# Kernel optimization log

Measured on AMD Instinct MI355X. Metric: run time of the kernel, lower is better.

## Reference

```python
import jax, jax.numpy as jnp
import numpy as np

INPUT_DIM = 256
RES_DIM = 2048
OUT_DIM = 256
BATCH = 32
SEQ = 512
LEAK = 0.3
TARGET_SR = 0.9
IN_CONN = 0.1
RES_CONN = 0.1
IN_SCALE = 1.0


def _make_params(seed=0):
    rng = np.random.default_rng(seed)
    W_in = rng.standard_normal((RES_DIM, INPUT_DIM)).astype(np.float32)
    W_in = W_in * (rng.random((RES_DIM, INPUT_DIM)) < IN_CONN).astype(np.float32) * IN_SCALE
    W = rng.standard_normal((RES_DIM, RES_DIM)).astype(np.float32)
    W = W * (rng.random((RES_DIM, RES_DIM)) < RES_CONN).astype(np.float32)
    sr = np.abs(np.linalg.eigvals(W.astype(np.float64))).max()
    if sr > 0:
        W = (W * (TARGET_SR / sr)).astype(np.float32)
    bias = np.zeros((RES_DIM,), np.float32)
    # readout Linear(reservoir_dim, output_dim), torch default init
    bound = 1.0 / np.sqrt(RES_DIM)
    w_ro = rng.uniform(-bound, bound, (OUT_DIM, RES_DIM)).astype(np.float32)
    b_ro = rng.uniform(-bound, bound, (OUT_DIM,)).astype(np.float32)
    return W_in, W, bias, w_ro, b_ro


def setup_inputs() -> dict:
    key = jax.random.key(0)
    k_u, _ = jax.random.split(key)
    u = jax.random.normal(k_u, (BATCH, SEQ, INPUT_DIM), dtype=jnp.float32)
    state = jnp.zeros((BATCH, RES_DIM), dtype=jnp.float32)
    W_in, W, bias, w_ro, b_ro = _make_params()
    return {
        'u': u,
        'state': state,
        'W_in': jnp.asarray(W_in),
        'W': jnp.asarray(W),
        'bias': jnp.asarray(bias),
        'w_ro': jnp.asarray(w_ro),
        'b_ro': jnp.asarray(b_ro),
    }


def reference(u, state, W_in, W, bias, w_ro, b_ro):
    # Precompute input projection for all timesteps in one GEMM: (T, B, R)
    u_proj = jnp.einsum('bti,ri->tbr', u, W_in) + bias

    def step(s, up):
        pre = up + s @ W.T            # (B, R)
        s = (1.0 - LEAK) * s + LEAK * jnp.tanh(pre)
        return s, s

    _, states = jax.lax.scan(step, state, u_proj)  # (T, B, R)
    states = jnp.transpose(states, (1, 0, 2))       # (B, T, R)
    output = jnp.einsum('btr,or->bto', states, w_ro) + b_ro
    return output
```

## Files before the change

kernel.cpp:

```cpp
#include <hip/hip_runtime.h>
#include <math.h>

#define BATCH 32
#define SEQ   512
#define IDIM  256
#define RDIM  2048
#define ODIM  256
#define LEAK  0.3f

#define SCAN_BLOCKS  256
#define SCAN_THREADS 512
#define ROWS_PER_BLK 8

typedef float f4 __attribute__((ext_vector_type(4)));

__device__ __forceinline__ unsigned ld_flag(const unsigned* p) {
    return __hip_atomic_load(p, __ATOMIC_RELAXED, __HIP_MEMORY_SCOPE_AGENT);
}
__device__ __forceinline__ void st_flag(unsigned* p, unsigned v) {
    __hip_atomic_store(p, v, __ATOMIC_RELAXED, __HIP_MEMORY_SCOPE_AGENT);
}

__global__ void esn_init(const float* __restrict__ s0, float* __restrict__ states,
                         unsigned* __restrict__ flags) {
    int idx = blockIdx.x * blockDim.x + threadIdx.x;
    const int n4 = (BATCH * RDIM) / 4;
    if (idx < n4) {
        ((float4*)states)[idx] = ((const float4*)s0)[idx];
    }
    if (idx < 512) flags[idx] = 0u;
}

#define UP_THREADS 256
__global__ __launch_bounds__(UP_THREADS) void esn_uproj(
    const float* __restrict__ u,
    const float* __restrict__ Win,
    const float* __restrict__ bias,
    float* __restrict__ up)
{
    __shared__ float St[32][68];
    __shared__ float Wt[32][68];

    const int tid  = threadIdx.x;
    const int row0 = blockIdx.x * 64;
    const int o0   = blockIdx.y * 64;

    const int lr = tid >> 3;
    const int lk = (tid & 7) * 4;
    const int tx = tid & 15;
    const int ty = tid >> 4;

    const int m0 = row0 + lr;
    const int m1 = row0 + 32 + lr;
    const float* u0 = u + ((size_t)(m0 & 31) * SEQ + (m0 >> 5)) * IDIM;
    const float* u1 = u + ((size_t)(m1 & 31) * SEQ + (m1 >> 5)) * IDIM;

    float acc[4][4] = {};

    for (int kt = 0; kt < IDIM; kt += 32) {
        float4 a0 = *(const float4*)(u0 + kt + lk);
        float4 a1 = *(const float4*)(u1 + kt + lk);
        float4 w0 = *(const float4*)(Win + (size_t)(o0 + lr)      * IDIM + kt + lk);
        float4 w1 = *(const float4*)(Win + (size_t)(o0 + 32 + lr) * IDIM + kt + lk);
        __syncthreads();
        float av0[4] = {a0.x, a0.y, a0.z, a0.w};
        float av1[4] = {a1.x, a1.y, a1.z, a1.w};
        float wv0[4] = {w0.x, w0.y, w0.z, w0.w};
        float wv1[4] = {w1.x, w1.y, w1.z, w1.w};
        #pragma unroll
        for (int j = 0; j < 4; ++j) {
            St[lk + j][lr]      = av0[j];
            St[lk + j][32 + lr] = av1[j];
            Wt[lk + j][lr]      = wv0[j];
            Wt[lk + j][32 + lr] = wv1[j];
        }
        __syncthreads();
        #pragma unroll
        for (int k = 0; k < 32; ++k) {
            float4 a4 = *(const float4*)(&St[k][4 * ty]);
            float4 b4 = *(const float4*)(&Wt[k][4 * tx]);
            float av[4] = {a4.x, a4.y, a4.z, a4.w};
            float bv[4] = {b4.x, b4.y, b4.z, b4.w};
            #pragma unroll
            for (int ri = 0; ri < 4; ++ri)
                #pragma unroll
                for (int oi = 0; oi < 4; ++oi)
                    acc[ri][oi] += av[ri] * bv[oi];
        }
    }

    float4 bs = *(const float4*)(bias + o0 + 4 * tx);
    float bsv[4] = {bs.x, bs.y, bs.z, bs.w};
    #pragma unroll
    for (int ri = 0; ri < 4; ++ri) {
        int row = row0 + 4 * ty + ri;
        float4 v;
        v.x = acc[ri][0] + bsv[0];
        v.y = acc[ri][1] + bsv[1];
        v.z = acc[ri][2] + bsv[2];
        v.w = acc[ri][3] + bsv[3];
        *(float4*)(up + (size_t)row * RDIM + o0 + 4 * tx) = v;
    }
}

#define DECL_A(r)  float A##r##0 = 0.0f, A##r##1 = 0.0f, A##r##2 = 0.0f, A##r##3 = 0.0f;
#define ZERO_A(r)  A##r##0 = 0.0f; A##r##1 = 0.0f; A##r##2 = 0.0f; A##r##3 = 0.0f;
#define DOT_ROW(r) { f4 w = *(const f4*)(wl + (r) * RDIM); \
    A##r##0 += w[0]*SC0[0] + w[1]*SC0[1] + w[2]*SC0[2] + w[3]*SC0[3]; \
    A##r##1 += w[0]*SC1[0] + w[1]*SC1[1] + w[2]*SC1[2] + w[3]*SC1[3]; \
    A##r##2 += w[0]*SC2[0] + w[1]*SC2[1] + w[2]*SC2[2] + w[3]*SC2[3]; \
    A##r##3 += w[0]*SC3[0] + w[1]*SC3[1] + w[2]*SC3[2] + w[3]*SC3[3]; }
#define RED12(x)   { x += __shfl_xor(x, 1, 64); x += __shfl_xor(x, 2, 64); }
#define RED_A(r)   RED12(A##r##0) RED12(A##r##1) RED12(A##r##2) RED12(A##r##3)
#define COMPACT(r) float V##r; { \
    float x01 = (q & 1) ? A##r##1 : A##r##0; \
    float x23 = (q & 1) ? A##r##3 : A##r##2; \
    float v   = (q & 2) ? x23 : x01; \
    v += __shfl_xor(v, 4, 64);  v += __shfl_xor(v, 8, 64); \
    v += __shfl_xor(v, 16, 64); v += __shfl_xor(v, 32, 64); \
    V##r = v; }

__global__ __launch_bounds__(SCAN_THREADS) void esn_scan(
    const float* __restrict__ W,
    float* __restrict__ states,
    unsigned* __restrict__ flags)
{
    __shared__ float Wl[ROWS_PER_BLK * RDIM];

    const int tid  = threadIdx.x;
    const int bid  = blockIdx.x;
    const int r0   = bid * ROWS_PER_BLK;
    unsigned* go   = flags + 320;

    {
        const float4* src = (const float4*)(W + (size_t)r0 * RDIM);
        float4* dst = (float4*)Wl;
        #pragma unroll
        for (int i = 0; i < (ROWS_PER_BLK * RDIM) / 4 / SCAN_THREADS; ++i)
            dst[i * SCAN_THREADS + tid] = src[i * SCAN_THREADS + tid];
    }

    const int wave = tid >> 6;
    const int lane = tid & 63;
    const int b0   = wave * 4;
    const int kb   = lane * 4;
    const int q    = lane & 3;

    const int bf = b0 + q;
    const int rr = lane >> 2;
    const size_t fin_off = (size_t)bf * RDIM + r0 + rr;

    float so = 0.0f;
    if (lane < 32) so = states[fin_off];

    DECL_A(0) DECL_A(1) DECL_A(2) DECL_A(3)
    DECL_A(4) DECL_A(5) DECL_A(6) DECL_A(7)

    __syncthreads();

    for (int t = 0; t < SEQ; ++t) {
        const float* prev = states + (size_t)t * (BATCH * RDIM);
        float* next = states + (size_t)(t + 1) * (BATCH * RDIM);

        float up = 0.0f;
        if (lane < 32)
            up = __hip_atomic_load(&next[fin_off], __ATOMIC_RELAXED,
                                   __HIP_MEMORY_SCOPE_AGENT);

        ZERO_A(0) ZERO_A(1) ZERO_A(2) ZERO_A(3)
        ZERO_A(4) ZERO_A(5) ZERO_A(6) ZERO_A(7)

        {
            const float* sb = prev + kb;
            f4 SC0 = *(const f4*)(sb + (size_t)(b0 + 0) * RDIM);
            f4 SC1 = *(const f4*)(sb + (size_t)(b0 + 1) * RDIM);
            f4 SC2 = *(const f4*)(sb + (size_t)(b0 + 2) * RDIM);
            f4 SC3 = *(const f4*)(sb + (size_t)(b0 + 3) * RDIM);

            #pragma unroll 1
            for (int c = 0; c < 8; ++c) {
                f4 SN0 = SC0, SN1 = SC1, SN2 = SC2, SN3 = SC3;
                if (c < 7) {
                    SN0 = *(const f4*)(sb + (size_t)(b0 + 0) * RDIM + (c + 1) * 256);
                    SN1 = *(const f4*)(sb + (size_t)(b0 + 1) * RDIM + (c + 1) * 256);
                    SN2 = *(const f4*)(sb + (size_t)(b0 + 2) * RDIM + (c + 1) * 256);
                    SN3 = *(const f4*)(sb + (size_t)(b0 + 3) * RDIM + (c + 1) * 256);
                }
                const float* wl = &Wl[c * 256 + kb];
                DOT_ROW(0) DOT_ROW(1) DOT_ROW(2) DOT_ROW(3)
                DOT_ROW(4) DOT_ROW(5) DOT_ROW(6) DOT_ROW(7)
                SC0 = SN0; SC1 = SN1; SC2 = SN2; SC3 = SN3;
            }
        }

        RED_A(0) RED_A(1) RED_A(2) RED_A(3)
        RED_A(4) RED_A(5) RED_A(6) RED_A(7)
        COMPACT(0) COMPACT(1) COMPACT(2) COMPACT(3)
        COMPACT(4) COMPACT(5) COMPACT(6) COMPACT(7)

        if (lane < 32) {
            float pre = V0;
            if (rr == 1) pre = V1;
            if (rr == 2) pre = V2;
            if (rr == 3) pre = V3;
            if (rr == 4) pre = V4;
            if (rr == 5) pre = V5;
            if (rr == 6) pre = V6;
            if (rr == 7) pre = V7;
            pre += up;
            float sn = (1.0f - LEAK) * so + LEAK * tanhf(pre);
            so = sn;
            __hip_atomic_store(&next[fin_off], sn,
                               __ATOMIC_RELAXED, __HIP_MEMORY_SCOPE_AGENT);
        }

        asm volatile("s_waitcnt vmcnt(0)" ::: "memory");
        __syncthreads();
        if (tid == 0) st_flag(&flags[bid], (unsigned)(t + 1));
        asm volatile("" ::: "memory");

        const unsigned tp = (unsigned)(t + 1);
        if (bid == 0) {
            if (tid < 64) {
                for (;;) {
                    unsigned f0 = ld_flag(&flags[tid]);
                    unsigned f1 = ld_flag(&flags[64 + tid]);
                    unsigned f2 = ld_flag(&flags[128 + tid]);
                    unsigned f3 = ld_flag(&flags[192 + tid]);
                    bool ok = (f0 >= tp) & (f1 >= tp) & (f2 >= tp) & (f3 >= tp);
                    if (__all(ok)) break;
                    __builtin_amdgcn_s_sleep(2);
                }
                asm volatile("" ::: "memory");
                if (tid == 0) st_flag(go, tp);
            }
        } else {
            if (tid == 0) {
                while (ld_flag(go) < tp) __builtin_amdgcn_s_sleep(2);
            }
        }
        __syncthreads();
    }
}

#define RO_THREADS 256
__global__ __launch_bounds__(RO_THREADS) void esn_readout(
    const float* __restrict__ states,
    const float* __restrict__ w_ro,
    const float* __restrict__ b_ro,
    float* __restrict__ out)
{
    __shared__ float St[32][68];
    __shared__ float Wt[32][68];

    const int tid  = threadIdx.x;
    const int rb   = blockIdx.x >> 2;
    const int ob   = blockIdx.x & 3;
    const int row0 = rb * 64;
    const int o0   = ob * 64;
    const float* S = states + (size_t)BATCH * RDIM;

    const int lr = tid >> 3;
    const int lk = (tid & 7) * 4;
    const int tx = tid & 15;
    const int ty = tid >> 4;

    float acc[4][4] = {};

    for (int kt = 0; kt < RDIM; kt += 32) {
        float4 a0 = *(const float4*)(S + (size_t)(row0 + lr)      * RDIM + kt + lk);
        float4 a1 = *(const float4*)(S + (size_t)(row0 + 32 + lr) * RDIM + kt + lk);
        float4 w0 = *(const float4*)(w_ro + (size_t)(o0 + lr)      * RDIM + kt + lk);
        float4 w1 = *(const float4*)(w_ro + (size_t)(o0 + 32 + lr) * RDIM + kt + lk);
        __syncthreads();
        float av0[4] = {a0.x, a0.y, a0.z, a0.w};
        float av1[4] = {a1.x, a1.y, a1.z, a1.w};
        float wv0[4] = {w0.x, w0.y, w0.z, w0.w};
        float wv1[4] = {w1.x, w1.y, w1.z, w1.w};
        #pragma unroll
        for (int j = 0; j < 4; ++j) {
            St[lk + j][lr]      = av0[j];
            St[lk + j][32 + lr] = av1[j];
            Wt[lk + j][lr]      = wv0[j];
            Wt[lk + j][32 + lr] = wv1[j];
        }
        __syncthreads();
        #pragma unroll
        for (int k = 0; k < 32; ++k) {
            float4 a4 = *(const float4*)(&St[k][4 * ty]);
            float4 b4 = *(const float4*)(&Wt[k][4 * tx]);
            float av[4] = {a4.x, a4.y, a4.z, a4.w};
            float bv[4] = {b4.x, b4.y, b4.z, b4.w};
            #pragma unroll
            for (int ri = 0; ri < 4; ++ri)
                #pragma unroll
                for (int oi = 0; oi < 4; ++oi)
                    acc[ri][oi] += av[ri] * bv[oi];
        }
    }

    float4 br = *(const float4*)(b_ro + o0 + 4 * tx);
    float brv[4] = {br.x, br.y, br.z, br.w};
    #pragma unroll
    for (int ri = 0; ri < 4; ++ri) {
        int row = row0 + 4 * ty + ri;
        int tt  = row >> 5;
        int bbx = row & 31;
        float4 v;
        v.x = acc[ri][0] + brv[0];
        v.y = acc[ri][1] + brv[1];
        v.z = acc[ri][2] + brv[2];
        v.w = acc[ri][3] + brv[3];
        *(float4*)(out + ((size_t)bbx * SEQ + tt) * ODIM + o0 + 4 * tx) = v;
    }
}

extern "C" void kernel_launch(void* const* d_in, const int* in_sizes, int n_in,
                              void* d_out, int out_size, void* d_ws, size_t ws_size,
                              hipStream_t stream) {
    const float* u    = (const float*)d_in[0];
    const float* s0   = (const float*)d_in[1];
    const float* Win  = (const float*)d_in[2];
    const float* W    = (const float*)d_in[3];
    const float* bias = (const float*)d_in[4];
    const float* w_ro = (const float*)d_in[5];
    const float* b_ro = (const float*)d_in[6];
    float* out = (float*)d_out;

    const size_t states_elems = (size_t)(SEQ + 1) * BATCH * RDIM;
    const size_t states_bytes = states_elems * sizeof(float);
    const size_t need = states_bytes + 2048;
    if (ws_size < need) return;

    float* states = (float*)d_ws;
    unsigned* flags = (unsigned*)((char*)d_ws + states_bytes);

    esn_init<<<dim3(64), dim3(256), 0, stream>>>(s0, states, flags);

    esn_uproj<<<dim3((SEQ * BATCH) / 64, RDIM / 64), dim3(UP_THREADS), 0, stream>>>(
        u, Win, bias, states + (size_t)BATCH * RDIM);

    void* args[] = { (void*)&W, (void*)&states, (void*)&flags };
    hipLaunchCooperativeKernel((const void*)esn_scan,
                               dim3(SCAN_BLOCKS), dim3(SCAN_THREADS),
                               args, 0, stream);

    esn_readout<<<dim3((SEQ * BATCH / 64) * (ODIM / 64)), dim3(RO_THREADS), 0, stream>>>(
        states, w_ro, b_ro, out);
}
```

Before: 5.010 ms.

## Split scan grid barrier into two independent batch-half groups with LDS counters

Replaces the per-step block-wide __syncthreads and single grid barrier with two separate barriers, one per group of four waves (each covering half the batch). Each group keeps its own global flag array, aggregator and go flag, and waves coordinate through LDS counters instead of __syncthreads. Because batches are independent, the two halves can proceed and synchronise separately, hiding part of the barrier latency and letting them overlap. This adds spin-waiting on LDS, more flag traffic, and a subtle cross-group coupling that limits how far the halves can drift apart.

Result: slower. 5.987 ms (+19.5%).

```diff
diff --git a/kernel.cpp b/kernel.cpp
--- a/kernel.cpp
+++ b/kernel.cpp
@@ -28,7 +28,7 @@
     if (idx < n4) {
         ((float4*)states)[idx] = ((const float4*)s0)[idx];
     }
-    if (idx < 512) flags[idx] = 0u;
+    if (idx < 1024) flags[idx] = 0u;
 }
 
 #define UP_THREADS 256
@@ -126,11 +126,13 @@
     unsigned* __restrict__ flags)
 {
     __shared__ float Wl[ROWS_PER_BLK * RDIM];
+    __shared__ unsigned lsync[32];
 
     const int tid  = threadIdx.x;
     const int bid  = blockIdx.x;
     const int r0   = bid * ROWS_PER_BLK;
-    unsigned* go   = flags + 320;
+
+    if (tid < 32) lsync[tid] = 0u;
 
     {
         const float4* src = (const float4*)(W + (size_t)r0 * RDIM);
@@ -142,6 +144,7 @@
 
     const int wave = tid >> 6;
     const int lane = tid & 63;
+    const int grp  = wave >> 2;
     const int b0   = wave * 4;
     const int kb   = lane * 4;
     const int q    = lane & 3;
@@ -150,6 +153,15 @@
     const int rr = lane >> 2;
     const size_t fin_off = (size_t)bf * RDIM + r0 + rr;
 
+    unsigned* myflag = flags + (grp ? 512 : 0) + bid;
+    unsigned* fbase  = flags + (grp ? 512 : 0);
+    unsigned* go     = flags + (grp ? 288 : 256);
+    volatile unsigned* cnt_mine  = (volatile unsigned*)&lsync[grp ? 8 : 0];
+    volatile unsigned* cnt_other = (volatile unsigned*)&lsync[grp ? 0 : 8];
+    volatile unsigned* gol       = (volatile unsigned*)&lsync[grp ? 24 : 16];
+    const bool is_relay = (wave == (grp ? 4 : 0));
+    const bool is_agg   = (bid == 0) && is_relay;
+
     float so = 0.0f;
     if (lane < 32) so = states[fin_off];
 
@@ -161,6 +173,13 @@
     for (int t = 0; t < SEQ; ++t) {
         const float* prev = states + (size_t)t * (BATCH * RDIM);
         float* next = states + (size_t)(t + 1) * (BATCH * RDIM);
+
+        while (*gol < (unsigned)t) __builtin_amdgcn_s_sleep(1);
+        {
+            const unsigned alt = 4u * (unsigned)t + (grp ? 4u : 0u);
+            while (*cnt_other < alt) __builtin_amdgcn_s_sleep(1);
+        }
+        asm volatile("" ::: "memory");
 
         float up = 0.0f;
         if (lane < 32)
@@ -215,31 +234,30 @@
         }
 
         asm volatile("s_waitcnt vmcnt(0)" ::: "memory");
-        __syncthreads();
-        if (tid == 0) st_flag(&flags[bid], (unsigned)(t + 1));
-        asm volatile("" ::: "memory");
-
         const unsigned tp = (unsigned)(t + 1);
-        if (bid == 0) {
-            if (tid < 64) {
-                for (;;) {
-                    unsigned f0 = ld_flag(&flags[tid]);
-                    unsigned f1 = ld_flag(&flags[64 + tid]);
-                    unsigned f2 = ld_flag(&flags[128 + tid]);
-                    unsigned f3 = ld_flag(&flags[192 + tid]);
-                    bool ok = (f0 >= tp) & (f1 >= tp) & (f2 >= tp) & (f3 >= tp);
-                    if (__all(ok)) break;
-                    __builtin_amdgcn_s_sleep(2);
-                }
-                asm volatile("" ::: "memory");
-                if (tid == 0) st_flag(go, tp);
+        if (lane == 0) {
+            unsigned old = atomicAdd((unsigned*)cnt_mine, 1u);
+            if (old == 4u * tp - 1u) st_flag(myflag, tp);
+        }
+
+        if (is_agg) {
+            for (;;) {
+                unsigned f0 = ld_flag(&fbase[lane]);
+                unsigned f1 = ld_flag(&fbase[64 + lane]);
+                unsigned f2 = ld_flag(&fbase[128 + lane]);
+                unsigned f3 = ld_flag(&fbase[192 + lane]);
+                bool ok = (f0 >= tp) & (f1 >= tp) & (f2 >= tp) & (f3 >= tp);
+                if (__all(ok)) break;
+                __builtin_amdgcn_s_sleep(2);
             }
-        } else {
-            if (tid == 0) {
+            asm volatile("" ::: "memory");
+            if (lane == 0) { st_flag(go, tp); *gol = tp; }
+        } else if (is_relay) {
+            if (lane == 0) {
                 while (ld_flag(go) < tp) __builtin_amdgcn_s_sleep(2);
+                *gol = tp;
             }
         }
-        __syncthreads();
     }
 }
 
@@ -329,7 +347,7 @@
 
     const size_t states_elems = (size_t)(SEQ + 1) * BATCH * RDIM;
     const size_t states_bytes = states_elems * sizeof(float);
-    const size_t need = states_bytes + 2048;
+    const size_t need = states_bytes + 4096;
     if (ws_size < need) return;
 
     float* states = (float*)d_ws;
```

## Replace block barriers with LDS wave counter and replicated per-wave go flags

Applied to the files above, without the earlier changes.

The per-timestep grid barrier no longer uses two __syncthreads per block. Each wave bumps a workgroup-scope LDS counter, and wave 0 publishes the block's flag once all 8 waves have arrived. The aggregator writes the go signal to 8 replicated flags spaced across cache lines, and every wave polls its assigned copy directly. This is meant to cut intra-block barrier latency and contention on a single go flag, at the cost of many more global pollers (every wave spins) and subtler memory-ordering guarantees.

After: 4.820 ms. 1.04x faster.

```diff
diff --git a/kernel.cpp b/kernel.cpp
--- a/kernel.cpp
+++ b/kernel.cpp
@@ -28,7 +28,7 @@
     if (idx < n4) {
         ((float4*)states)[idx] = ((const float4*)s0)[idx];
     }
-    if (idx < 512) flags[idx] = 0u;
+    if (idx < 1024) flags[idx] = 0u;
 }
 
 #define UP_THREADS 256
@@ -126,11 +126,13 @@
     unsigned* __restrict__ flags)
 {
     __shared__ float Wl[ROWS_PER_BLK * RDIM];
+    __shared__ unsigned lcnt;
 
     const int tid  = threadIdx.x;
     const int bid  = blockIdx.x;
     const int r0   = bid * ROWS_PER_BLK;
-    unsigned* go   = flags + 320;
+
+    if (tid == 0) lcnt = 0u;
 
     {
         const float4* src = (const float4*)(W + (size_t)r0 * RDIM);
@@ -149,6 +151,9 @@
     const int bf = b0 + q;
     const int rr = lane >> 2;
     const size_t fin_off = (size_t)bf * RDIM + r0 + rr;
+
+    unsigned* mygo = &flags[256 + (bid & 7) * 16];
+    const bool is_agg = (bid == 0) && (wave == 0);
 
     float so = 0.0f;
     if (lane < 32) so = states[fin_off];
@@ -215,31 +220,36 @@
         }
 
         asm volatile("s_waitcnt vmcnt(0)" ::: "memory");
-        __syncthreads();
-        if (tid == 0) st_flag(&flags[bid], (unsigned)(t + 1));
-        asm volatile("" ::: "memory");
-
         const unsigned tp = (unsigned)(t + 1);
-        if (bid == 0) {
-            if (tid < 64) {
+        if (lane == 0) __hip_atomic_fetch_add(&lcnt, 1u, __ATOMIC_RELAXED,
+                                              __HIP_MEMORY_SCOPE_WORKGROUP);
+
+        if (wave == 0) {
+            if (lane == 0) {
+                while (__hip_atomic_load(&lcnt, __ATOMIC_RELAXED,
+                                         __HIP_MEMORY_SCOPE_WORKGROUP) < 8u * tp)
+                    __builtin_amdgcn_s_sleep(1);
+                st_flag(&flags[bid], tp);
+            }
+            if (is_agg) {
                 for (;;) {
-                    unsigned f0 = ld_flag(&flags[tid]);
-                    unsigned f1 = ld_flag(&flags[64 + tid]);
-                    unsigned f2 = ld_flag(&flags[128 + tid]);
-                    unsigned f3 = ld_flag(&flags[192 + tid]);
+                    unsigned f0 = ld_flag(&flags[lane]);
+                    unsigned f1 = ld_flag(&flags[64 + lane]);
+                    unsigned f2 = ld_flag(&flags[128 + lane]);
+                    unsigned f3 = ld_flag(&flags[192 + lane]);
                     bool ok = (f0 >= tp) & (f1 >= tp) & (f2 >= tp) & (f3 >= tp);
                     if (__all(ok)) break;
-                    __builtin_amdgcn_s_sleep(2);
+                    __builtin_amdgcn_s_sleep(1);
                 }
                 asm volatile("" ::: "memory");
-                if (tid == 0) st_flag(go, tp);
+                if (lane < 8) st_flag(&flags[256 + lane * 16], tp);
+                asm volatile("s_waitcnt vmcnt(0)" ::: "memory");
+                continue;
             }
-        } else {
-            if (tid == 0) {
-                while (ld_flag(go) < tp) __builtin_amdgcn_s_sleep(2);
-            }
-        }
-        __syncthreads();
+        }
+
+        while (ld_flag(mygo) < tp) __builtin_amdgcn_s_sleep(1);
+        asm volatile("" ::: "memory");
     }
 }
 
@@ -329,7 +339,7 @@
 
     const size_t states_elems = (size_t)(SEQ + 1) * BATCH * RDIM;
     const size_t states_bytes = states_elems * sizeof(float);
-    const size_t need = states_bytes + 2048;
+    const size_t need = states_bytes + 4096;
     if (ws_size < need) return;
 
     float* states = (float*)d_ws;
```
